# Kernel optimization log

Measured on AMD Instinct MI355X. Metric: run time of the kernel, lower is better.

Reference implementation:

```python
import jax, jax.numpy as jnp
import numpy as np

D_MODEL = 512
NUM_HEADS = 8


def setup_inputs() -> dict:
    key = jax.random.key(0)
    ks = jax.random.split(key, 6)
    B, S, D = 4, 2048, D_MODEL
    Q = jax.random.normal(ks[0], (B, S, D), dtype=jnp.float32)
    K = jax.random.normal(ks[1], (B, S, D), dtype=jnp.float32)
    V = jax.random.normal(ks[2], (B, S, D), dtype=jnp.float32)
    # boolean mask, True = masked out; random so no row is fully masked
    mask = jax.random.randint(ks[3], (B, S, S), 0, 2).astype(jnp.bool_)
    scale = 1.0 / np.sqrt(D)
    Wq = jax.random.normal(ks[4], (D, D), dtype=jnp.float32) * scale
    Wo = jax.random.normal(ks[5], (D, D), dtype=jnp.float32) * scale
    return {"Q": Q, "K": K, "V": V, "mask": mask, "Wq": Wq, "Wo": Wo}


def reference(Q, K, V, mask, Wq, Wo):
    B, S, D = Q.shape
    H = NUM_HEADS
    dk = D // H
    # Faithful to the source: Q_Linear's weight (Wq) is applied to Q, K AND V
    # (K_Linear / V_Linear are dead parameters in the original module).
    q = (Q @ Wq.T).reshape(B, S, H, dk)
    k = (K @ Wq.T).reshape(B, S, H, dk)
    v = (V @ Wq.T).reshape(B, S, H, dk)
    # scores: [B, H, Sq, Sk]
    scores = jnp.einsum("bqhd,bkhd->bhqk", q, k)
    scores = jnp.where(mask[:, None, :, :], -jnp.inf, scores)
    w = jax.nn.softmax(scores / jnp.sqrt(jnp.asarray(dk, scores.dtype)), axis=-1)
    c = jnp.einsum("bhqk,bkhd->bqhd", w, v).reshape(B, S, D)
    return c @ Wo.T
```

## Files before the change

kernel.cpp:

```cpp
#include <hip/hip_runtime.h>
#include <math.h>

#define B_ 4
#define S_ 2048
#define D_ 512
#define H_ 8
#define DK_ 64
#define MROWS (B_ * S_)

typedef short bf16x8 __attribute__((ext_vector_type(8)));
typedef short bf16x4 __attribute__((ext_vector_type(4)));
typedef float f32x4 __attribute__((ext_vector_type(4)));
typedef float f32x16 __attribute__((ext_vector_type(16)));

static __device__ __forceinline__ unsigned short f2bf(float x) {
    unsigned int u = __float_as_uint(x);
    return (unsigned short)((u + 0x7FFFu + ((u >> 16) & 1u)) >> 16);
}
static __device__ __forceinline__ unsigned int cvt_pk_bf16(float a, float b) {
    unsigned int r;
    asm("v_cvt_pk_bf16_f32 %0, %1, %2" : "=v"(r) : "v"(a), "v"(b));
    return r;
}
static __device__ __forceinline__ float exp2_fast(float x) {
    float r;
    asm("v_exp_f32 %0, %1" : "=v"(r) : "v"(x));
    return r;
}
static __device__ __forceinline__ void gld_lds16(const unsigned short* g, unsigned short* l) {
    __builtin_amdgcn_global_load_lds(
        (const __attribute__((address_space(1))) unsigned int*)g,
        (__attribute__((address_space(3))) unsigned int*)l, 16, 0, 0);
}
static __device__ __forceinline__ void plswap(unsigned int& a, unsigned int& b) {
    asm volatile("v_permlane32_swap_b32 %0, %1" : "+v"(a), "+v"(b));
}

#define NXE (MROWS * D_)
#define NWE (D_ * D_)
#define CAST_BLOCKS ((3 * NXE + 2 * NWE) / 8 / 256)
#define MASK_BLOCKS (B_ * S_ * S_ / 256)

__global__ __launch_bounds__(256) void prep(const float* __restrict__ Q,
                                            const float* __restrict__ K,
                                            const float* __restrict__ V,
                                            const float* __restrict__ Wq,
                                            const float* __restrict__ Wo,
                                            const void* __restrict__ mask,
                                            unsigned short* __restrict__ Qb,
                                            unsigned short* __restrict__ Kb,
                                            unsigned short* __restrict__ Vb,
                                            unsigned short* __restrict__ Wqb,
                                            unsigned short* __restrict__ Wob,
                                            unsigned long long* __restrict__ mb) {
    if (blockIdx.x < CAST_BLOCKS) {
        const int NA = NXE / 8;
        const int NWn = NWE / 8;
        int id = blockIdx.x * 256 + threadIdx.x;
        const float* src;
        unsigned short* dst;
        if (id < 3 * NA) {
            int a = id / NA, r = id - a * NA;
            src = (a == 0 ? Q : a == 1 ? K : V) + (size_t)r * 8;
            dst = (a == 0 ? Qb : a == 1 ? Kb : Vb) + (size_t)r * 8;
        } else {
            int r = id - 3 * NA;
            int a = r / NWn; r -= a * NWn;
            src = (a == 0 ? Wq : Wo) + (size_t)r * 8;
            dst = (a == 0 ? Wqb : Wob) + (size_t)r * 8;
        }
        float4 x = *(const float4*)src;
        float4 y = *(const float4*)(src + 4);
        unsigned short u[8] = {f2bf(x.x), f2bf(x.y), f2bf(x.z), f2bf(x.w),
                               f2bf(y.x), f2bf(y.y), f2bf(y.z), f2bf(y.w)};
        *(uint4*)dst = *(const uint4*)u;
    } else {
        const int id = (blockIdx.x - CAST_BLOCKS) * 256 + threadIdx.x;
        unsigned int accw = 0;
        if ((threadIdx.x & 63) == 0) {
            const unsigned int* mw0 = (const unsigned int*)mask;
            #pragma unroll
            for (int i = 0; i < 16; ++i) accw |= mw0[i];
        }
        accw = __shfl(accw, 0);
        const bool bytemode = (accw & 0xFFFFFF00u) != 0u;
        int val;
        if (bytemode) val = ((const unsigned char*)mask)[id];
        else          val = ((const int*)mask)[id];
        unsigned long long w = __ballot(val != 0);
        if ((threadIdx.x & 63) == 0) mb[id >> 6] = w;
    }
}

__global__ __launch_bounds__(256) void proj3(const unsigned short* __restrict__ Qb,
                                             const unsigned short* __restrict__ Kb,
                                             const unsigned short* __restrict__ Vb,
                                             const unsigned short* __restrict__ Wqb,
                                             unsigned short* __restrict__ qs,
                                             unsigned short* __restrict__ kbo,
                                             unsigned short* __restrict__ vt) {
    __shared__ unsigned short As[128 * 40];
    __shared__ unsigned short Bs[128 * 40];
    const int t = threadIdx.x;
    const int w = t >> 6, lane = t & 63, col = lane & 15, quad = lane >> 4;
    const int bm = blockIdx.x * 128, bn = blockIdx.y * 128;
    const int z = blockIdx.z;
    const unsigned short* X = (z == 0) ? Qb : (z == 1) ? Kb : Vb;
    const int wm = (w >> 1) * 64, wn = (w & 1) * 64;
    const int srow = t >> 1, shalf = t & 1;

    const unsigned short* xg = X + (size_t)(bm + srow) * D_ + shalf * 16;
    const unsigned short* wg = Wqb + (size_t)(bn + srow) * D_ + shalf * 16;
    unsigned short* asw = &As[srow * 40 + shalf * 16];
    unsigned short* bsw = &Bs[srow * 40 + shalf * 16];

    f32x4 acc[4][4];
    #pragma unroll
    for (int i = 0; i < 4; ++i)
        #pragma unroll
        for (int j = 0; j < 4; ++j) acc[i][j] = (f32x4){0.f, 0.f, 0.f, 0.f};

    #pragma unroll 1
    for (int k0 = 0; k0 < D_; k0 += 32) {
        __syncthreads();
        {
            uint4 a0 = *(const uint4*)(xg + k0);
            uint4 a1 = *(const uint4*)(xg + k0 + 8);
            uint4 b0 = *(const uint4*)(wg + k0);
            uint4 b1 = *(const uint4*)(wg + k0 + 8);
            *(uint4*)asw = a0; *(uint4*)(asw + 8) = a1;
            *(uint4*)bsw = b0; *(uint4*)(bsw + 8) = b1;
        }
        __syncthreads();

        bf16x8 af[4], bg[4];
        #pragma unroll
        for (int i = 0; i < 4; ++i)
            af[i] = *(const bf16x8*)&As[(wm + i * 16 + col) * 40 + quad * 8];
        #pragma unroll
        for (int j = 0; j < 4; ++j)
            bg[j] = *(const bf16x8*)&Bs[(wn + j * 16 + col) * 40 + quad * 8];
        #pragma unroll
        for (int i = 0; i < 4; ++i)
            #pragma unroll
            for (int j = 0; j < 4; ++j)
                acc[i][j] = __builtin_amdgcn_mfma_f32_16x16x32_bf16(
                    af[i], bg[j], acc[i][j], 0, 0, 0);
    }

    if (z == 2) {
        #pragma unroll
        for (int i = 0; i < 4; ++i) {
            const int R = bm + wm + i * 16 + quad * 4;
            const int bb = R >> 11, s0 = R & (S_ - 1);
            #pragma unroll
            for (int j = 0; j < 4; ++j) {
                const int C = bn + wn + j * 16 + col;
                const int hh = C >> 6, dd = C & (DK_ - 1);
                ushort4 u = make_ushort4(f2bf(acc[i][j][0]), f2bf(acc[i][j][1]),
                                         f2bf(acc[i][j][2]), f2bf(acc[i][j][3]));
                *(ushort4*)&vt[(((size_t)bb * H_ + hh) * DK_ + dd) * S_ + s0] = u;
            }
        }
    } else {
        unsigned short* O = (z == 0) ? qs : kbo;
        const float scl = (z == 0) ? 0.18033688f : 1.0f;
        #pragma unroll
        for (int i = 0; i < 4; ++i)
            #pragma unroll
            for (int j = 0; j < 4; ++j) {
                const int R = bm + wm + i * 16 + quad * 4;
                const int C = bn + wn + j * 16 + col;
                #pragma unroll
                for (int r = 0; r < 4; ++r)
                    O[(size_t)(R + r) * D_ + C] = f2bf(acc[i][j][r] * scl);
            }
    }
}

__global__ __launch_bounds__(256) void gemm_out(const unsigned short* __restrict__ Xb,
                                                const unsigned short* __restrict__ Wob,
                                                float* __restrict__ Out) {
    __shared__ unsigned short As[128 * 40];
    __shared__ unsigned short Bs[128 * 40];
    const int t = threadIdx.x;
    const int w = t >> 6, lane = t & 63, col = lane & 15, quad = lane >> 4;
    const int bm = blockIdx.x * 128, bn = blockIdx.y * 128;
    const int wm = (w >> 1) * 64, wn = (w & 1) * 64;
    const int srow = t >> 1, shalf = t & 1;

    const unsigned short* xg = Xb + (size_t)(bm + srow) * D_ + shalf * 16;
    const unsigned short* wg = Wob + (size_t)(bn + srow) * D_ + shalf * 16;
    unsigned short* asw = &As[srow * 40 + shalf * 16];
    unsigned short* bsw = &Bs[srow * 40 + shalf * 16];

    f32x4 acc[4][4];
    #pragma unroll
    for (int i = 0; i < 4; ++i)
        #pragma unroll
        for (int j = 0; j < 4; ++j) acc[i][j] = (f32x4){0.f, 0.f, 0.f, 0.f};

    #pragma unroll 1
    for (int k0 = 0; k0 < D_; k0 += 32) {
        __syncthreads();
        {
            uint4 a0 = *(const uint4*)(xg + k0);
            uint4 a1 = *(const uint4*)(xg + k0 + 8);
            uint4 b0 = *(const uint4*)(wg + k0);
            uint4 b1 = *(const uint4*)(wg + k0 + 8);
            *(uint4*)asw = a0; *(uint4*)(asw + 8) = a1;
            *(uint4*)bsw = b0; *(uint4*)(bsw + 8) = b1;
        }
        __syncthreads();

        bf16x8 af[4], bg[4];
        #pragma unroll
        for (int i = 0; i < 4; ++i)
            af[i] = *(const bf16x8*)&As[(wm + i * 16 + col) * 40 + quad * 8];
        #pragma unroll
        for (int j = 0; j < 4; ++j)
            bg[j] = *(const bf16x8*)&Bs[(wn + j * 16 + col) * 40 + quad * 8];
        #pragma unroll
        for (int i = 0; i < 4; ++i)
            #pragma unroll
            for (int j = 0; j < 4; ++j)
                acc[i][j] = __builtin_amdgcn_mfma_f32_16x16x32_bf16(
                    af[i], bg[j], acc[i][j], 0, 0, 0);
    }

    #pragma unroll
    for (int i = 0; i < 4; ++i)
        #pragma unroll
        for (int j = 0; j < 4; ++j) {
            const int R = bm + wm + i * 16 + quad * 4;
            const int C = bn + wn + j * 16 + col;
            #pragma unroll
            for (int r = 0; r < 4; ++r)
                Out[(size_t)(R + r) * D_ + C] = acc[i][j][r];
        }
}

__global__ __launch_bounds__(256, 4) void attn_mfma(
        const unsigned short* __restrict__ qb,
        const unsigned short* __restrict__ kb,
        const unsigned short* __restrict__ vt,
        const unsigned long long* __restrict__ mb,
        unsigned short* __restrict__ o0,
        unsigned short* __restrict__ o1,
        float* __restrict__ l0,
        float* __restrict__ l1) {
    __shared__ unsigned short sm[16384];
    const int t = threadIdx.x;
    const int w = t >> 6;
    const int lane = t & 63;
    const int q5 = lane & 31;
    const int hi = lane >> 5;
    const int h = blockIdx.y;
    const int b = blockIdx.z >> 1;
    const int khalf = blockIdx.z & 1;
    const int bh = b * H_ + h;
    const int qrow0 = blockIdx.x * 128 + w * 32;

    unsigned short* opart = khalf ? o1 : o0;
    float* lpart = khalf ? l1 : l0;

    const unsigned int chk = cvt_pk_bf16(1.0f, 2.0f);
    const bool ablow = ((chk & 0xFFFFu) == 0x3F80u);

    bf16x8 qf[4];
    {
        const unsigned short* qp =
            qb + (size_t)(b * S_ + qrow0 + q5) * D_ + h * DK_ + hi * 8;
        #pragma unroll
        for (int dsl = 0; dsl < 4; ++dsl)
            qf[dsl] = *(const bf16x8*)(qp + dsl * 16);
    }

    bf16x8 ones8;
    #pragma unroll
    for (int i = 0; i < 8; ++i) ones8[i] = (short)0x3F80;

    f32x16 Oa, Ob, lacc;
    #pragma unroll
    for (int i = 0; i < 16; ++i) { Oa[i] = 0.f; Ob[i] = 0.f; lacc[i] = 0.f; }

    const float CREF = 8.656170245f;
    const int kbeg = khalf * (S_ / 2);

    const int ln8 = lane >> 3;
    const int fs8 = ((lane & 7) ^ ln8) * 8;
    const int r0 = w * 16 + ln8;
    const unsigned short* pK0 = kb + (size_t)(b * S_ + kbeg + r0) * D_ + h * DK_ + fs8;
    const unsigned short* pK1 = pK0 + 8 * D_;
    const unsigned short* pV0 = vt + ((size_t)bh * DK_ + r0) * S_ + kbeg + fs8;
    const unsigned short* pV1 = pV0 + 8 * S_;

    const unsigned long long* mbase =
        mb + (size_t)(b * S_ + qrow0 + q5) * (S_ / 64) + (kbeg >> 6);

    gld_lds16(pK0, &sm[w * 1024]);
    gld_lds16(pK1, &sm[w * 1024 + 512]);
    gld_lds16(pV0, &sm[4096 + w * 1024]);
    gld_lds16(pV1, &sm[4096 + w * 1024 + 512]);
    pK0 += 64 * D_; pK1 += 64 * D_; pV0 += 64; pV1 += 64;

    const int x7 = (q5 & 7);

    #pragma unroll 1
    for (int ti = 0; ti < 16; ++ti) {
        unsigned long long mw = mbase[ti];
        __builtin_amdgcn_sched_barrier(0);
        if (ti < 15) {
            const int nb = (ti & 1) ? 0 : 8192;
            gld_lds16(pK0, &sm[nb + w * 1024]);
            gld_lds16(pK1, &sm[nb + w * 1024 + 512]);
            gld_lds16(pV0, &sm[nb + 4096 + w * 1024]);
            gld_lds16(pV1, &sm[nb + 4096 + w * 1024 + 512]);
            pK0 += 64 * D_; pK1 += 64 * D_; pV0 += 64; pV1 += 64;
            __asm__ __volatile__("s_waitcnt vmcnt(5)" ::: "memory");
        } else {
            __asm__ __volatile__("s_waitcnt vmcnt(1)" ::: "memory");
        }
        __builtin_amdgcn_s_barrier();

        const int KB = (ti & 1) ? 8192 : 0;
        const int VB = KB + 4096;
        const unsigned long long msh = mw >> (hi * 4);

        #pragma unroll
        for (int kbi = 0; kbi < 2; ++kbi) {
            const int krow = KB + (kbi * 32 + q5) * 64;
            f32x16 S;
            #pragma unroll
            for (int i = 0; i < 16; ++i) S[i] = 0.f;
            __builtin_amdgcn_s_setprio(1);
            #pragma unroll
            for (int dsl = 0; dsl < 4; ++dsl) {
                bf16x8 kf = *(const bf16x8*)&sm[krow + (((dsl << 1) | hi) ^ x7) * 8];
                S = __builtin_amdgcn_mfma_f32_32x32x16_bf16(kf, qf[dsl], S, 0, 0, 0);
            }
            __builtin_amdgcn_s_setprio(0);

            float p[16];
            #pragma unroll
            for (int r = 0; r < 16; ++r) {
                const int c = kbi * 32 + (r & 3) + 8 * (r >> 2);
                const bool msk = ((msh >> c) & 1ull) != 0ull;
                p[r] = exp2_fast((msk ? -1e30f : S[r]) - CREF);
            }

            #pragma unroll
            for (int ksl = 0; ksl < 2; ++ksl) {
                const int bsl = ksl * 8;
                unsigned int uA = ablow ? cvt_pk_bf16(p[bsl], p[bsl + 1])
                                        : cvt_pk_bf16(p[bsl + 1], p[bsl]);
                unsigned int uB = ablow ? cvt_pk_bf16(p[bsl + 2], p[bsl + 3])
                                        : cvt_pk_bf16(p[bsl + 3], p[bsl + 2]);
                unsigned int uC = ablow ? cvt_pk_bf16(p[bsl + 4], p[bsl + 5])
                                        : cvt_pk_bf16(p[bsl + 5], p[bsl + 4]);
                unsigned int uD = ablow ? cvt_pk_bf16(p[bsl + 6], p[bsl + 7])
                                        : cvt_pk_bf16(p[bsl + 7], p[bsl + 6]);
                plswap(uA, uC);
                plswap(uB, uD);
                union { unsigned int u[4]; bf16x8 v; } pa;
                pa.u[0] = uA; pa.u[1] = uB; pa.u[2] = uC; pa.u[3] = uD;

                const int slice = kbi * 2 + ksl;
                const int vseg = (((slice << 1) | hi) ^ x7) * 8;
                bf16x8 vf0 = *(const bf16x8*)&sm[VB + q5 * 64 + vseg];
                bf16x8 vf1 = *(const bf16x8*)&sm[VB + (32 + q5) * 64 + vseg];
                __builtin_amdgcn_s_setprio(1);
                lacc = __builtin_amdgcn_mfma_f32_32x32x16_bf16(pa.v, ones8, lacc, 0, 0, 0);
                Oa = __builtin_amdgcn_mfma_f32_32x32x16_bf16(pa.v, vf0, Oa, 0, 0, 0);
                Ob = __builtin_amdgcn_mfma_f32_32x32x16_bf16(pa.v, vf1, Ob, 0, 0, 0);
                __builtin_amdgcn_s_setprio(0);
            }
        }

        __builtin_amdgcn_s_barrier();
    }

    #pragma unroll
    for (int r = 0; r < 16; ++r) {
        const int qq = (r & 3) + 8 * (r >> 2) + 4 * hi;
        const size_t row = (size_t)(b * S_ + qrow0 + qq);
        opart[row * D_ + h * DK_ + q5]      = f2bf(Oa[r]);
        opart[row * D_ + h * DK_ + 32 + q5] = f2bf(Ob[r]);
        if (q5 == 0) lpart[row * H_ + h] = lacc[r];
    }
}

__global__ __launch_bounds__(256) void combine(const unsigned short* __restrict__ o0,
                                               const unsigned short* __restrict__ o1,
                                               const float* __restrict__ l0,
                                               const float* __restrict__ l1,
                                               unsigned short* __restrict__ cb) {
    const int id = blockIdx.x * 256 + threadIdx.x;
    const size_t base = (size_t)id * 8;
    const int row = (int)(base >> 9);
    const int hh = ((int)base & (D_ - 1)) >> 6;
    uint4 ua = *(const uint4*)(o0 + base);
    uint4 ub = *(const uint4*)(o1 + base);
    const float inv = 1.0f / (l0[(size_t)row * H_ + hh] + l1[(size_t)row * H_ + hh]);
    const unsigned short* pa = (const unsigned short*)&ua;
    const unsigned short* pb = (const unsigned short*)&ub;
    unsigned short out[8];
    #pragma unroll
    for (int i = 0; i < 8; ++i) {
        float fa = __uint_as_float((unsigned int)pa[i] << 16);
        float fb = __uint_as_float((unsigned int)pb[i] << 16);
        out[i] = f2bf((fa + fb) * inv);
    }
    *(uint4*)(cb + base) = *(const uint4*)out;
}

extern "C" void kernel_launch(void* const* d_in, const int* in_sizes, int n_in,
                              void* d_out, int out_size, void* d_ws, size_t ws_size,
                              hipStream_t stream) {
    const float* Q    = (const float*)d_in[0];
    const float* K    = (const float*)d_in[1];
    const float* V    = (const float*)d_in[2];
    const void*  mask = d_in[3];
    const float* Wq   = (const float*)d_in[4];
    const float* Wo   = (const float*)d_in[5];
    float* out = (float*)d_out;

    const size_t NX = (size_t)MROWS * D_;
    const size_t NW = (size_t)D_ * D_;
    unsigned short* Qb   = (unsigned short*)d_ws;
    unsigned short* Kb   = Qb + NX;
    unsigned short* Vb   = Kb + NX;
    unsigned short* Wqb  = Vb + NX;
    unsigned short* Wob  = Wqb + NW;
    unsigned short* qbuf = Wob + NW;
    unsigned short* kbuf = qbuf + NX;
    unsigned short* vtb  = kbuf + NX;
    unsigned short* cbuf = vtb + NX;
    unsigned long long* mb = (unsigned long long*)(cbuf + NX);

    unsigned short* o0 = Qb;
    unsigned short* o1 = Kb;
    float* l0 = (float*)Vb;
    float* l1 = l0 + (size_t)MROWS * H_;

    prep<<<dim3(CAST_BLOCKS + MASK_BLOCKS), dim3(256), 0, stream>>>(
        Q, K, V, Wq, Wo, mask, Qb, Kb, Vb, Wqb, Wob, mb);

    proj3<<<dim3(MROWS / 128, D_ / 128, 3), dim3(256), 0, stream>>>(
        Qb, Kb, Vb, Wqb, qbuf, kbuf, vtb);

    attn_mfma<<<dim3(S_ / 128, H_, B_ * 2), dim3(256), 0, stream>>>(
        qbuf, kbuf, vtb, mb, o0, o1, l0, l1);

    combine<<<dim3((int)(NX / 8 / 256)), dim3(256), 0, stream>>>(o0, o1, l0, l1, cbuf);

    gemm_out<<<dim3(MROWS / 128, D_ / 128), dim3(256), 0, stream>>>(cbuf, Wob, out);
}
```

Baseline: 281.0 us.

## Double-buffer GEMM tiles with direct global-to-LDS loads and XOR swizzle

```diff
diff --git a/kernel.cpp b/kernel.cpp
--- a/kernel.cpp
+++ b/kernel.cpp
@@ -9,7 +9,6 @@
 #define MROWS (B_ * S_)
 
 typedef short bf16x8 __attribute__((ext_vector_type(8)));
-typedef short bf16x4 __attribute__((ext_vector_type(4)));
 typedef float f32x4 __attribute__((ext_vector_type(4)));
 typedef float f32x16 __attribute__((ext_vector_type(16)));
 
@@ -99,20 +98,19 @@
                                              unsigned short* __restrict__ qs,
                                              unsigned short* __restrict__ kbo,
                                              unsigned short* __restrict__ vt) {
-    __shared__ unsigned short As[128 * 40];
-    __shared__ unsigned short Bs[128 * 40];
+    __shared__ unsigned short smx[16384];
     const int t = threadIdx.x;
     const int w = t >> 6, lane = t & 63, col = lane & 15, quad = lane >> 4;
     const int bm = blockIdx.x * 128, bn = blockIdx.y * 128;
     const int z = blockIdx.z;
     const unsigned short* X = (z == 0) ? Qb : (z == 1) ? Kb : Vb;
     const int wm = (w >> 1) * 64, wn = (w & 1) * 64;
-    const int srow = t >> 1, shalf = t & 1;
-
-    const unsigned short* xg = X + (size_t)(bm + srow) * D_ + shalf * 16;
-    const unsigned short* wg = Wqb + (size_t)(bn + srow) * D_ + shalf * 16;
-    unsigned short* asw = &As[srow * 40 + shalf * 16];
-    unsigned short* bsw = &Bs[srow * 40 + shalf * 16];
+
+    const int sr = w * 32 + (lane >> 2);
+    const int ssw = (((lane & 3) ^ ((lane >> 3) & 3)) * 8);
+    const unsigned short* ags = X + (size_t)(bm + sr) * D_ + ssw;
+    const unsigned short* bgs = Wqb + (size_t)(bn + sr) * D_ + ssw;
+    const int pseg = ((quad ^ ((col >> 1) & 3)) * 8);
 
     f32x4 acc[4][4];
     #pragma unroll
@@ -120,32 +118,43 @@
         #pragma unroll
         for (int j = 0; j < 4; ++j) acc[i][j] = (f32x4){0.f, 0.f, 0.f, 0.f};
 
+    gld_lds16(ags, &smx[w * 1024]);
+    gld_lds16(ags + 16 * D_, &smx[w * 1024 + 512]);
+    gld_lds16(bgs, &smx[4096 + w * 1024]);
+    gld_lds16(bgs + 16 * D_, &smx[4096 + w * 1024 + 512]);
+    __asm__ __volatile__("s_waitcnt vmcnt(0)" ::: "memory");
+    __builtin_amdgcn_s_barrier();
+
+    int cur = 0;
     #pragma unroll 1
     for (int k0 = 0; k0 < D_; k0 += 32) {
-        __syncthreads();
-        {
-            uint4 a0 = *(const uint4*)(xg + k0);
-            uint4 a1 = *(const uint4*)(xg + k0 + 8);
-            uint4 b0 = *(const uint4*)(wg + k0);
-            uint4 b1 = *(const uint4*)(wg + k0 + 8);
-            *(uint4*)asw = a0; *(uint4*)(asw + 8) = a1;
-            *(uint4*)bsw = b0; *(uint4*)(bsw + 8) = b1;
-        }
-        __syncthreads();
-
+        if (k0 + 32 < D_) {
+            const int nb = (cur ^ 1) * 8192;
+            gld_lds16(ags + k0 + 32, &smx[nb + w * 1024]);
+            gld_lds16(ags + 16 * D_ + k0 + 32, &smx[nb + w * 1024 + 512]);
+            gld_lds16(bgs + k0 + 32, &smx[nb + 4096 + w * 1024]);
+            gld_lds16(bgs + 16 * D_ + k0 + 32, &smx[nb + 4096 + w * 1024 + 512]);
+        }
+        __builtin_amdgcn_sched_barrier(0);
+
+        const int cb = cur * 8192;
         bf16x8 af[4], bg[4];
         #pragma unroll
         for (int i = 0; i < 4; ++i)
-            af[i] = *(const bf16x8*)&As[(wm + i * 16 + col) * 40 + quad * 8];
+            af[i] = *(const bf16x8*)&smx[cb + (wm + i * 16 + col) * 32 + pseg];
         #pragma unroll
         for (int j = 0; j < 4; ++j)
-            bg[j] = *(const bf16x8*)&Bs[(wn + j * 16 + col) * 40 + quad * 8];
+            bg[j] = *(const bf16x8*)&smx[cb + 4096 + (wn + j * 16 + col) * 32 + pseg];
         #pragma unroll
         for (int i = 0; i < 4; ++i)
             #pragma unroll
             for (int j = 0; j < 4; ++j)
                 acc[i][j] = __builtin_amdgcn_mfma_f32_16x16x32_bf16(
                     af[i], bg[j], acc[i][j], 0, 0, 0);
+
+        __asm__ __volatile__("s_waitcnt vmcnt(0)" ::: "memory");
+        __builtin_amdgcn_s_barrier();
+        cur ^= 1;
     }
 
     if (z == 2) {
@@ -181,18 +190,17 @@
 __global__ __launch_bounds__(256) void gemm_out(const unsigned short* __restrict__ Xb,
                                                 const unsigned short* __restrict__ Wob,
                                                 float* __restrict__ Out) {
-    __shared__ unsigned short As[128 * 40];
-    __shared__ unsigned short Bs[128 * 40];
+    __shared__ unsigned short smx[16384];
     const int t = threadIdx.x;
     const int w = t >> 6, lane = t & 63, col = lane & 15, quad = lane >> 4;
     const int bm = blockIdx.x * 128, bn = blockIdx.y * 128;
     const int wm = (w >> 1) * 64, wn = (w & 1) * 64;
-    const int srow = t >> 1, shalf = t & 1;
-
-    const unsigned short* xg = Xb + (size_t)(bm + srow) * D_ + shalf * 16;
-    const unsigned short* wg = Wob + (size_t)(bn + srow) * D_ + shalf * 16;
-    unsigned short* asw = &As[srow * 40 + shalf * 16];
-    unsigned short* bsw = &Bs[srow * 40 + shalf * 16];
+
+    const int sr = w * 32 + (lane >> 2);
+    const int ssw = (((lane & 3) ^ ((lane >> 3) & 3)) * 8);
+    const unsigned short* ags = Xb + (size_t)(bm + sr) * D_ + ssw;
+    const unsigned short* bgs = Wob + (size_t)(bn + sr) * D_ + ssw;
+    const int pseg = ((quad ^ ((col >> 1) & 3)) * 8);
 
     f32x4 acc[4][4];
     #pragma unroll
@@ -200,32 +208,43 @@
         #pragma unroll
         for (int j = 0; j < 4; ++j) acc[i][j] = (f32x4){0.f, 0.f, 0.f, 0.f};
 
+    gld_lds16(ags, &smx[w * 1024]);
+    gld_lds16(ags + 16 * D_, &smx[w * 1024 + 512]);
+    gld_lds16(bgs, &smx[4096 + w * 1024]);
+    gld_lds16(bgs + 16 * D_, &smx[4096 + w * 1024 + 512]);
+    __asm__ __volatile__("s_waitcnt vmcnt(0)" ::: "memory");
+    __builtin_amdgcn_s_barrier();
+
+    int cur = 0;
     #pragma unroll 1
     for (int k0 = 0; k0 < D_; k0 += 32) {
-        __syncthreads();
-        {
-            uint4 a0 = *(const uint4*)(xg + k0);
-            uint4 a1 = *(const uint4*)(xg + k0 + 8);
-            uint4 b0 = *(const uint4*)(wg + k0);
-            uint4 b1 = *(const uint4*)(wg + k0 + 8);
-            *(uint4*)asw = a0; *(uint4*)(asw + 8) = a1;
-            *(uint4*)bsw = b0; *(uint4*)(bsw + 8) = b1;
-        }
-        __syncthreads();
-
+        if (k0 + 32 < D_) {
+            const int nb = (cur ^ 1) * 8192;
+            gld_lds16(ags + k0 + 32, &smx[nb + w * 1024]);
+            gld_lds16(ags + 16 * D_ + k0 + 32, &smx[nb + w * 1024 + 512]);
+            gld_lds16(bgs + k0 + 32, &smx[nb + 4096 + w * 1024]);
+            gld_lds16(bgs + 16 * D_ + k0 + 32, &smx[nb + 4096 + w * 1024 + 512]);
+        }
+        __builtin_amdgcn_sched_barrier(0);
+
+        const int cb = cur * 8192;
         bf16x8 af[4], bg[4];
         #pragma unroll
         for (int i = 0; i < 4; ++i)
-            af[i] = *(const bf16x8*)&As[(wm + i * 16 + col) * 40 + quad * 8];
+            af[i] = *(const bf16x8*)&smx[cb + (wm + i * 16 + col) * 32 + pseg];
         #pragma unroll
         for (int j = 0; j < 4; ++j)
-            bg[j] = *(const bf16x8*)&Bs[(wn + j * 16 + col) * 40 + quad * 8];
+            bg[j] = *(const bf16x8*)&smx[cb + 4096 + (wn + j * 16 + col) * 32 + pseg];
         #pragma unroll
         for (int i = 0; i < 4; ++i)
             #pragma unroll
             for (int j = 0; j < 4; ++j)
                 acc[i][j] = __builtin_amdgcn_mfma_f32_16x16x32_bf16(
                     af[i], bg[j], acc[i][j], 0, 0, 0);
+
+        __asm__ __volatile__("s_waitcnt vmcnt(0)" ::: "memory");
+        __builtin_amdgcn_s_barrier();
+        cur ^= 1;
     }
 
     #pragma unroll
```

New measurement: 266.4 us. 1.05x faster.
